# Kernel optimization log

Measured on AMD Instinct MI355X. Metric: run time of the kernel, lower is better.

Reference implementation:

```python
import jax, jax.numpy as jnp
import numpy as np

T, B, V, E, H = 256, 64, 10000, 400, 1152


def _n(k, shape, scale=0.05):
    return jax.random.normal(k, shape, jnp.float32) * scale


def setup_inputs() -> dict:
    key = jax.random.key(0)
    ks = jax.random.split(key, 32)
    inp = {}
    inp["x"] = jax.random.randint(ks[0], (T, B), 0, V)
    inp["h0"] = _n(ks[1], (B, H)); inp["h1"] = _n(ks[2], (B, H)); inp["h2"] = _n(ks[3], (B, E))
    inp["c0"] = _n(ks[4], (B, H)); inp["c1"] = _n(ks[5], (B, H)); inp["c2"] = _n(ks[6], (B, E))
    inp["emb"] = _n(ks[7], (V, E), 0.1)
    # layer i: (input_dim, output_dim): (E,H), (H,H), (H,E)
    sizes = [(E, H), (H, H), (H, E)]
    j = 8
    for i, (din, dout) in enumerate(sizes):
        inp[f"W_ih{i}"] = _n(ks[j], (4 * dout, din)); j += 1
        inp[f"W_hh{i}"] = _n(ks[j], (4 * dout, dout)); j += 1
        inp[f"b_ih{i}"] = _n(ks[j], (4 * dout,)); j += 1
        inp[f"b_hh{i}"] = _n(ks[j], (4 * dout,)); j += 1
    inp["dec_W"] = _n(ks[j], (V, E)); j += 1
    inp["dec_b"] = jnp.zeros((V,), jnp.float32)
    return inp


def lstm_cell(x, h, c, Wih, Whh, bih, bhh):
    # PyTorch LSTMCell: gates = x@Wih^T + bih + h@Whh^T + bhh, order i,f,g,o
    g = x @ Wih.T + h @ Whh.T + bih + bhh
    i, f, gg, o = jnp.split(g, 4, axis=-1)
    c2 = jax.nn.sigmoid(f) * c + jax.nn.sigmoid(i) * jnp.tanh(gg)
    h2 = jax.nn.sigmoid(o) * jnp.tanh(c2)
    return h2, c2


def reference(x, h0, h1, h2, c0, c1, c2, emb,
              W_ih0, W_hh0, b_ih0, b_hh0,
              W_ih1, W_hh1, b_ih1, b_hh1,
              W_ih2, W_hh2, b_ih2, b_hh2,
              dec_W, dec_b):
    xe = emb[x]  # [T, B, E]

    def step(carry, xt):
        a0, a1, a2, s0, s1, s2 = carry
        a0, s0 = lstm_cell(xt, a0, s0, W_ih0, W_hh0, b_ih0, b_hh0)
        a1, s1 = lstm_cell(a0, a1, s1, W_ih1, W_hh1, b_ih1, b_hh1)
        a2, s2 = lstm_cell(a1, a2, s2, W_ih2, W_hh2, b_ih2, b_hh2)
        return (a0, a1, a2, s0, s1, s2), a2

    _, out = jax.lax.scan(step, (h0, h1, h2, c0, c1, c2), xe)  # out: [T, B, E]
    decoded = out @ dec_W.T + dec_b  # [T, B, V]
    return decoded
```

## Files before the change

### kernel.cpp

```cpp
#include <hip/hip_runtime.h>
#include <hip/hip_bf16.h>

typedef __hip_bfloat16 bf16;
typedef __attribute__((ext_vector_type(8))) short short8;
typedef __attribute__((ext_vector_type(4))) float f32x4;

#define T_ 256
#define B_ 64
#define V_ 10000
#define E_ 400
#define H_ 1152
#define KU 2304
#define XW 416
#define KD 416
#define XET (XW*B_)
#define NBLK 169

#define MFMA16 __builtin_amdgcn_mfma_f32_16x16x32_bf16
#define ATL(p) __hip_atomic_load((p), __ATOMIC_RELAXED, __HIP_MEMORY_SCOPE_AGENT)
#define ATS(p, v) __hip_atomic_store((p), (v), __ATOMIC_RELAXED, __HIP_MEMORY_SCOPE_AGENT)
#define PIN(x) asm volatile("" : "+v"(x))


__global__ __launch_bounds__(256) void prep_wint(
    const float* __restrict__ s1, int w1,
    const float* __restrict__ s2, int off2, int w2, int Hl,
    bf16* __restrict__ dst, long total)
{
    long i = (long)blockIdx.x * 256 + threadIdx.x;
    if (i >= total) return;
    int r = (int)(i / KU), k = (int)(i % KU);
    int hcol = r >> 2, gate = r & 3;
    long srow = (long)gate * Hl + hcol;
    float v = 0.f;
    if (k < w1) v = s1[srow * w1 + k];
    else if (k >= off2 && k < off2 + w2) v = s2[srow * w2 + (k - off2)];
    dst[i] = __float2bfloat16(v);
}

__global__ __launch_bounds__(256) void prep_wcat(
    const float* __restrict__ s1, int w1,
    bf16* __restrict__ dst, int Ktot, long total)
{
    long i = (long)blockIdx.x * 256 + threadIdx.x;
    if (i >= total) return;
    int k = (int)(i % Ktot);
    long n = i / Ktot;
    dst[i] = __float2bfloat16(k < w1 ? s1[n * w1 + k] : 0.f);
}

__global__ __launch_bounds__(256) void bias_int(
    const float* __restrict__ a, const float* __restrict__ b,
    int Hl, float* __restrict__ d, int n)
{
    int r = blockIdx.x * 256 + threadIdx.x;
    if (r >= n) return;
    int hcol = r >> 2, gate = r & 3;
    d[r] = a[gate * Hl + hcol] + b[gate * Hl + hcol];
}

__global__ __launch_bounds__(256) void gather_xef(
    const int* __restrict__ x, const float* __restrict__ emb,
    bf16* __restrict__ XEf)
{
    long i = (long)blockIdx.x * 256 + threadIdx.x;
    if (i >= (long)T_ * B_ * XW) return;
    int k = (int)(i % XW);
    int b = (int)((i / XW) % B_);
    int t = (int)(i / ((long)XW * B_));
    float v = (k < E_) ? emb[(long)x[t * B_ + b] * E_ + k] : 0.f;
    XEf[(long)t * XET + (((k >> 3) * 64 + b) << 3) + (k & 7)] = __float2bfloat16(v);
}

__global__ __launch_bounds__(256) void copy_hf(
    const float* __restrict__ src, bf16* __restrict__ dst, int cols, int total)
{
    int i = blockIdx.x * 256 + threadIdx.x;
    if (i >= total) return;
    int k = i % cols, b = i / cols;
    dst[(((k >> 3) * 64 + b) << 3) + (k & 7)] = __float2bfloat16(src[(long)b * cols + k]);
}

__global__ __launch_bounds__(256) void copy_f32(
    const float* __restrict__ src, float* __restrict__ dst, int n)
{
    int i = blockIdx.x * 256 + threadIdx.x;
    if (i < n) dst[i] = src[i];
}

__device__ __forceinline__ void grid_bar(int* flags, int* gen, int phase) {
    asm volatile("s_waitcnt vmcnt(0)" ::: "memory");
    __syncthreads();
    if (blockIdx.x == 0) {
        if (threadIdx.x < 64) {
            const int ln = threadIdx.x;
            if (ln == 0) ATS(&flags[0], phase);
            for (;;) {
                int f0 = (ln       < NBLK) ? ATL(&flags[ln])       : phase;
                int f1 = (ln + 64  < NBLK) ? ATL(&flags[ln + 64])  : phase;
                int f2 = (ln + 128 < NBLK) ? ATL(&flags[ln + 128]) : phase;
                if (__all(f0 >= phase && f1 >= phase && f2 >= phase)) break;
                __builtin_amdgcn_s_sleep(1);
            }
            if (ln == 0) {
                ATS(gen, phase);
                __builtin_amdgcn_fence(__ATOMIC_ACQUIRE, "agent");
            }
        }
    } else {
        if (threadIdx.x == 0) {
            ATS(&flags[blockIdx.x], phase);
            while (ATL(gen) < phase)
                __builtin_amdgcn_s_sleep(1);
            __builtin_amdgcn_fence(__ATOMIC_ACQUIRE, "agent");
        }
    }
    __syncthreads();
    asm volatile("" ::: "memory");
}

struct Frag4 { short8 f0, f1, f2, f3; };

__global__ __launch_bounds__(512, 2) void awd_persistent(
    const bf16* __restrict__ XEf,
    const bf16* __restrict__ W0, const bf16* __restrict__ W1, const bf16* __restrict__ W2,
    const float* __restrict__ b0, const float* __restrict__ b1, const float* __restrict__ b2,
    bf16* H0f0, bf16* H0f1, bf16* H1f0, bf16* H1f1, bf16* H2f0, bf16* H2f1,
    float* c0, float* c1, float* c2, bf16* OUTB,
    int* flags, int* gen)
{
    __shared__ float gsm[2][4][64][65];
    __shared__ unsigned short hsm[64][24];
    const int bid = blockIdx.x;
    const int tid = threadIdx.x;
    const int lane = tid & 63;
    const int w8 = tid >> 6;
    const int lh = lane >> 4, l15 = lane & 15;
    const int boff8 = (lh * 64 + l15) * 8;

    int layer, grp;
    if (bid < 72)       { layer = 1; grp = bid; }
    else if (bid < 144) { layer = 0; grp = bid - 72; }
    else                { layer = 2; grp = bid - 144; }

    const bf16* Wp  = (layer == 0) ? W0 : (layer == 1) ? W1 : W2;
    const float* bias = (layer == 0) ? b0 : (layer == 1) ? b1 : b2;
    const float* cbuf = (layer == 0) ? c0 : (layer == 1) ? c1 : c2;
    const int Hl  = (layer == 2) ? 400 : 1152;
    const int bkt = (layer == 0) ? 13 : 36;
    const int nkt = (layer == 1) ? 72 : 49;
    const int KT  = (layer == 1) ? 9  : 7;
    const int kbase = w8 * KT;

    short8 wreg[9][4];
    #pragma unroll
    for (int u = 0; u < 9; ++u)
        if (u < KT) {
            #pragma unroll
            for (int rt = 0; rt < 4; ++rt) {
                int row = grp * 64 + rt * 16 + l15;
                int k   = (kbase + u) * 32 + lh * 8;
                wreg[u][rt] = *(const short8*)(Wp + (long)row * KU + k);
                PIN(wreg[u][rt]);
            }
        }

    float myb[2][4];
    #pragma unroll
    for (int e = 0; e < 2; ++e)
        #pragma unroll
        for (int g = 0; g < 4; ++g)
            myb[e][g] = bias[grp * 64 + (w8 + e * 8) * 4 + g];

    float creg[2];
    #pragma unroll
    for (int e = 0; e < 2; ++e)
        creg[e] = cbuf[(long)lane * Hl + grp * 16 + w8 + e * 8];

    for (int s = -1; s <= 256; ++s) {
        bool active = (layer == 0) ? (s <= 254)
                    : (layer == 1) ? (s >= 0 && s <= 255)
                                   : (s >= 1);
        if (active) {
            const int p = s & 1, q = p ^ 1;
            const bf16 *A1, *A2; bf16* hfW; bf16* ob = nullptr;
            if (layer == 0) {
                A1 = XEf + (long)(s + 1) * XET;
                A2 = p ? H0f1 : H0f0;
                hfW = q ? H0f1 : H0f0;
            } else if (layer == 1) {
                A1 = p ? H0f1 : H0f0;
                A2 = q ? H1f1 : H1f0;
                hfW = p ? H1f1 : H1f0;
            } else {
                A1 = q ? H1f1 : H1f0;
                A2 = p ? H2f1 : H2f0;
                hfW = q ? H2f1 : H2f0;
                ob = OUTB + (long)(s - 1) * B_ * XW;
            }

            auto loadf = [&](int u) -> Frag4 {
                const int ktg = kbase + u;
                const bf16* src; int ktL;
                if (ktg < bkt)      { src = A1; ktL = ktg; }
                else if (ktg < nkt) { src = A2; ktL = ktg - bkt; }
                else                { src = A1; ktL = 0; }
                const bf16* pB = src + ktL * 2048 + boff8;
                Frag4 r;
                r.f0 = *(const short8*)(pB);
                r.f1 = *(const short8*)(pB + 128);
                r.f2 = *(const short8*)(pB + 256);
                r.f3 = *(const short8*)(pB + 384);
                return r;
            };

            f32x4 acc[4][4];
            #pragma unroll
            for (int rt = 0; rt < 4; ++rt)
                #pragma unroll
                for (int m = 0; m < 4; ++m)
                    acc[rt][m] = (f32x4){0.f, 0.f, 0.f, 0.f};

            auto domfma = [&](int u, const Frag4& f) {
                #pragma unroll
                for (int rt = 0; rt < 4; ++rt) {
                    acc[rt][0] = MFMA16(wreg[u][rt], f.f0, acc[rt][0], 0, 0, 0);
                    acc[rt][1] = MFMA16(wreg[u][rt], f.f1, acc[rt][1], 0, 0, 0);
                    acc[rt][2] = MFMA16(wreg[u][rt], f.f2, acc[rt][2], 0, 0, 0);
                    acc[rt][3] = MFMA16(wreg[u][rt], f.f3, acc[rt][3], 0, 0, 0);
                }
            };

            #pragma unroll
            for (int u = 0; u < 9; ++u)
                if (u < KT) {
                    Frag4 f = loadf(u);
                    domfma(u, f);
                }

            #pragma unroll
            for (int rt = 0; rt < 4; ++rt)
                #pragma unroll
                for (int m = 0; m < 4; ++m)
                    #pragma unroll
                    for (int r = 0; r < 4; ++r)
                        gsm[w8 >> 2][w8 & 3][rt * 16 + lh * 4 + r][m * 16 + l15] = acc[rt][m][r];
            __syncthreads();

            #pragma unroll
            for (int e = 0; e < 2; ++e) {
                int b = lane;
                int cl = w8 + e * 8;
                float gv[4];
                #pragma unroll
                for (int g = 0; g < 4; ++g) {
                    float v = myb[e][g];
                    #pragma unroll
                    for (int kq = 0; kq < 4; ++kq)
                        v += gsm[0][kq][cl * 4 + g][b] + gsm[1][kq][cl * 4 + g][b];
                    gv[g] = v;
                }
                float c_old = creg[e];
                float i_s = 1.f / (1.f + expf(-gv[0]));
                float f_s = 1.f / (1.f + expf(-gv[1]));
                float o_s = 1.f / (1.f + expf(-gv[3]));
                float c_new = f_s * c_old + i_s * tanhf(gv[2]);
                float hval = o_s * tanhf(c_new);
                creg[e] = c_new;
                bf16 hb = __float2bfloat16(hval);
                unsigned short hbits;
                __builtin_memcpy(&hbits, &hb, 2);
                hsm[b][cl] = hbits;
            }
            __syncthreads();

            if (w8 < 2) {
                unsigned long long v0, v1;
                __builtin_memcpy(&v0, &hsm[lane][w8 * 8], 8);
                __builtin_memcpy(&v1, &hsm[lane][w8 * 8 + 4], 8);
                unsigned long long* qp =
                    (unsigned long long*)(hfW + (((long)grp * 2 + w8) * 64 + lane) * 8);
                ATS(qp, v0);
                ATS(qp + 1, v1);
            } else if (w8 == 2 && layer == 2) {
                short8 v0 = *(const short8*)&hsm[lane][0];
                short8 v1 = *(const short8*)&hsm[lane][8];
                *(short8*)(ob + (long)lane * XW + grp * 16) = v0;
                *(short8*)(ob + (long)lane * XW + grp * 16 + 8) = v1;
            }
        }
        grid_bar(flags, gen, s + 2);
    }
}

__global__ __launch_bounds__(256) void decoder(
    const bf16* __restrict__ A, const bf16* __restrict__ W,
    const float* __restrict__ bias, float* __restrict__ out)
{
    const int tid = threadIdx.x;
    const int lane = tid & 63;
    const int w = tid >> 6;
    const int mw = w >> 1, nw = w & 1;
    const int n0 = blockIdx.x * 128 + nw * 64;
    const int m0 = blockIdx.y * 128 + mw * 64;
    const int c16 = lane & 15;
    const int kg = lane >> 4;

    f32x4 acc[4][4];
    #pragma unroll
    for (int mi = 0; mi < 4; ++mi)
        #pragma unroll
        for (int ns = 0; ns < 4; ++ns)
            acc[mi][ns] = (f32x4){0.f, 0.f, 0.f, 0.f};

    int nrow[4];
    #pragma unroll
    for (int ns = 0; ns < 4; ++ns) {
        int n = n0 + ns * 16 + c16;
        nrow[ns] = (n < V_) ? n : (V_ - 1);
    }

    const bf16* arow = A + (long)(m0 + c16) * KD + kg * 8;
    #pragma unroll
    for (int kt = 0; kt < 13; ++kt) {
        short8 af[4], bf[4];
        #pragma unroll
        for (int mi = 0; mi < 4; ++mi)
            af[mi] = *(const short8*)(arow + (long)mi * 16 * KD + kt * 32);
        #pragma unroll
        for (int ns = 0; ns < 4; ++ns)
            bf[ns] = *(const short8*)(W + (long)nrow[ns] * KD + kt * 32 + kg * 8);
        #pragma unroll
        for (int mi = 0; mi < 4; ++mi)
            #pragma unroll
            for (int ns = 0; ns < 4; ++ns)
                acc[mi][ns] = MFMA16(af[mi], bf[ns], acc[mi][ns], 0, 0, 0);
    }

    #pragma unroll
    for (int mi = 0; mi < 4; ++mi)
        #pragma unroll
        for (int ns = 0; ns < 4; ++ns) {
            int col = n0 + ns * 16 + c16;
            if (col < V_) {
                float bv = bias[col];
                #pragma unroll
                for (int r = 0; r < 4; ++r) {
                    int row = m0 + mi * 16 + kg * 4 + r;
                    out[(size_t)row * V_ + col] = acc[mi][ns][r] + bv;
                }
            }
        }
}


extern "C" void kernel_launch(void* const* d_in, const int* in_sizes, int n_in,
                              void* d_out, int out_size, void* d_ws, size_t ws_size,
                              hipStream_t stream)
{
    const int*   x    = (const int*)d_in[0];
    const float* h0   = (const float*)d_in[1];
    const float* h1   = (const float*)d_in[2];
    const float* h2   = (const float*)d_in[3];
    const float* c0   = (const float*)d_in[4];
    const float* c1   = (const float*)d_in[5];
    const float* c2   = (const float*)d_in[6];
    const float* emb  = (const float*)d_in[7];
    const float* Wih0 = (const float*)d_in[8];
    const float* Whh0 = (const float*)d_in[9];
    const float* bih0 = (const float*)d_in[10];
    const float* bhh0 = (const float*)d_in[11];
    const float* Wih1 = (const float*)d_in[12];
    const float* Whh1 = (const float*)d_in[13];
    const float* bih1 = (const float*)d_in[14];
    const float* bhh1 = (const float*)d_in[15];
    const float* Wih2 = (const float*)d_in[16];
    const float* Whh2 = (const float*)d_in[17];
    const float* bih2 = (const float*)d_in[18];
    const float* bhh2 = (const float*)d_in[19];
    const float* decW = (const float*)d_in[20];
    const float* decb = (const float*)d_in[21];

    char* wsb = (char*)d_ws;
    size_t off = 0;
    auto alloc = [&](size_t bytes) -> void* {
        void* ptr = wsb + off;
        off = (off + bytes + 255) & ~(size_t)255;
        return ptr;
    };

    bf16* W0i = (bf16*)alloc((size_t)4608 * KU * 2);
    bf16* W1i = (bf16*)alloc((size_t)4608 * KU * 2);
    bf16* W2i = (bf16*)alloc((size_t)1600 * KU * 2);
    bf16* Wdc = (bf16*)alloc((size_t)V_ * KD * 2);
    float* b0i = (float*)alloc(4608 * 4);
    float* b1i = (float*)alloc(4608 * 4);
    float* b2i = (float*)alloc(1600 * 4);
    bf16* XEf = (bf16*)alloc((size_t)T_ * XET * 2);
    bf16* H0f0 = (bf16*)alloc((size_t)B_ * H_ * 2);
    bf16* H0f1 = (bf16*)alloc((size_t)B_ * H_ * 2);
    bf16* H1f0 = (bf16*)alloc((size_t)B_ * H_ * 2);
    bf16* H1f1 = (bf16*)alloc((size_t)B_ * H_ * 2);
    bf16* H2f0 = (bf16*)alloc((size_t)B_ * XW * 2);
    bf16* H2f1 = (bf16*)alloc((size_t)B_ * XW * 2);
    float* c0b = (float*)alloc((size_t)B_ * H_ * 4);
    float* c1b = (float*)alloc((size_t)B_ * H_ * 4);
    float* c2b = (float*)alloc((size_t)B_ * E_ * 4);
    bf16* OUTB = (bf16*)alloc((size_t)T_ * B_ * XW * 2);
    int* gbar = (int*)alloc(2048);

    auto cdiv = [](long a, long b) { return (int)((a + b - 1) / b); };

    hipMemsetAsync(gbar, 0, 2048, stream);

    prep_wint<<<cdiv(4608L * KU, 256), 256, 0, stream>>>(Wih0, 400,  Whh0, 416,  1152, 1152, W0i, 4608L * KU);
    prep_wint<<<cdiv(4608L * KU, 256), 256, 0, stream>>>(Wih1, 1152, Whh1, 1152, 1152, 1152, W1i, 4608L * KU);
    prep_wint<<<cdiv(1600L * KU, 256), 256, 0, stream>>>(Wih2, 1152, Whh2, 1152, 400,  400,  W2i, 1600L * KU);
    prep_wcat<<<cdiv((long)V_ * KD, 256), 256, 0, stream>>>(decW, 400, Wdc, KD, (long)V_ * KD);
    bias_int<<<cdiv(4608, 256), 256, 0, stream>>>(bih0, bhh0, 1152, b0i, 4608);
    bias_int<<<cdiv(4608, 256), 256, 0, stream>>>(bih1, bhh1, 1152, b1i, 4608);
    bias_int<<<cdiv(1600, 256), 256, 0, stream>>>(bih2, bhh2, 400,  b2i, 1600);
    gather_xef<<<cdiv((long)T_ * B_ * XW, 256), 256, 0, stream>>>(x, emb, XEf);

    hipMemsetAsync(H2f0, 0, (size_t)B_ * XW * 2, stream);
    hipMemsetAsync(H2f1, 0, (size_t)B_ * XW * 2, stream);
    hipMemsetAsync(OUTB, 0, (size_t)T_ * B_ * XW * 2, stream);

    copy_hf<<<cdiv(B_ * H_, 256), 256, 0, stream>>>(h0, H0f1, H_, B_ * H_);
    copy_hf<<<cdiv(B_ * H_, 256), 256, 0, stream>>>(h1, H1f1, H_, B_ * H_);
    copy_hf<<<cdiv(B_ * E_, 256), 256, 0, stream>>>(h2, H2f1, E_, B_ * E_);
    copy_f32<<<cdiv(B_ * H_, 256), 256, 0, stream>>>(c0, c0b, B_ * H_);
    copy_f32<<<cdiv(B_ * H_, 256), 256, 0, stream>>>(c1, c1b, B_ * H_);
    copy_f32<<<cdiv(B_ * E_, 256), 256, 0, stream>>>(c2, c2b, B_ * E_);

    {
        int* flags = gbar;
        int* gen   = gbar + 448;
        void* args[] = {
            (void*)&XEf, (void*)&W0i, (void*)&W1i, (void*)&W2i,
            (void*)&b0i, (void*)&b1i, (void*)&b2i,
            (void*)&H0f0, (void*)&H0f1, (void*)&H1f0, (void*)&H1f1,
            (void*)&H2f0, (void*)&H2f1,
            (void*)&c0b, (void*)&c1b, (void*)&c2b, (void*)&OUTB,
            (void*)&flags, (void*)&gen
        };
        hipLaunchCooperativeKernel((void*)awd_persistent, dim3(NBLK), dim3(512),
                                   args, 0, stream);
    }

    decoder<<<dim3((V_ + 127) / 128, (T_ * B_) / 128), 256, 0, stream>>>(
        OUTB, Wdc, decb, (float*)d_out);
}
```

Before: 3.157 ms.

## Replace global grid barrier with per-layer group flags and triple-buffered hidden states

Drops the single grid-wide barrier, which made every step wait for all 169 blocks. Each layer group now has a leader that collects its blocks' flags and publishes a per-layer generation counter. Blocks wait only on the layer counters they depend on, so layers can drift up to a step apart. To make that slack safe, hidden-state buffers go from double to triple buffering with a rotating read/write index. The cost is more polling and trickier ordering, and correctness depends on the dependency offsets and buffer rotation lining up.

```diff
diff --git a/kernel.cpp b/kernel.cpp
--- a/kernel.cpp
+++ b/kernel.cpp
@@ -88,46 +88,21 @@
     if (i < n) dst[i] = src[i];
 }
 
-__device__ __forceinline__ void grid_bar(int* flags, int* gen, int phase) {
-    asm volatile("s_waitcnt vmcnt(0)" ::: "memory");
-    __syncthreads();
-    if (blockIdx.x == 0) {
-        if (threadIdx.x < 64) {
-            const int ln = threadIdx.x;
-            if (ln == 0) ATS(&flags[0], phase);
-            for (;;) {
-                int f0 = (ln       < NBLK) ? ATL(&flags[ln])       : phase;
-                int f1 = (ln + 64  < NBLK) ? ATL(&flags[ln + 64])  : phase;
-                int f2 = (ln + 128 < NBLK) ? ATL(&flags[ln + 128]) : phase;
-                if (__all(f0 >= phase && f1 >= phase && f2 >= phase)) break;
-                __builtin_amdgcn_s_sleep(1);
-            }
-            if (ln == 0) {
-                ATS(gen, phase);
-                __builtin_amdgcn_fence(__ATOMIC_ACQUIRE, "agent");
-            }
-        }
-    } else {
-        if (threadIdx.x == 0) {
-            ATS(&flags[blockIdx.x], phase);
-            while (ATL(gen) < phase)
-                __builtin_amdgcn_s_sleep(1);
-            __builtin_amdgcn_fence(__ATOMIC_ACQUIRE, "agent");
-        }
-    }
-    __syncthreads();
-    asm volatile("" ::: "memory");
-}
-
 struct Frag4 { short8 f0, f1, f2, f3; };
+
+__device__ __forceinline__ void wait_ge(int* p, int v) {
+    while (ATL(p) < v) __builtin_amdgcn_s_sleep(1);
+}
 
 __global__ __launch_bounds__(512, 2) void awd_persistent(
     const bf16* __restrict__ XEf,
     const bf16* __restrict__ W0, const bf16* __restrict__ W1, const bf16* __restrict__ W2,
     const float* __restrict__ b0, const float* __restrict__ b1, const float* __restrict__ b2,
-    bf16* H0f0, bf16* H0f1, bf16* H1f0, bf16* H1f1, bf16* H2f0, bf16* H2f1,
+    bf16* H0a, bf16* H0b, bf16* H0c,
+    bf16* H1a, bf16* H1b, bf16* H1c,
+    bf16* H2a, bf16* H2b, bf16* H2c,
     float* c0, float* c1, float* c2, bf16* OUTB,
-    int* flags, int* gen)
+    int* flags, int* gd)
 {
     __shared__ float gsm[2][4][64][65];
     __shared__ unsigned short hsm[64][24];
@@ -143,6 +118,10 @@
     else if (bid < 144) { layer = 0; grp = bid - 72; }
     else                { layer = 2; grp = bid - 144; }
 
+    const bool isLeader = (bid == 0 || bid == 72 || bid == 144);
+    const int gbase = (layer == 1) ? 0 : (layer == 0) ? 72 : 144;
+    const int gcnt  = (layer == 2) ? 25 : 72;
+
     const bf16* Wp  = (layer == 0) ? W0 : (layer == 1) ? W1 : W2;
     const float* bias = (layer == 0) ? b0 : (layer == 1) ? b1 : b2;
     const float* cbuf = (layer == 0) ? c0 : (layer == 1) ? c1 : c2;
@@ -177,25 +156,40 @@
     for (int e = 0; e < 2; ++e)
         creg[e] = cbuf[(long)lane * Hl + grp * 16 + w8 + e * 8];
 
+    int rb = 0;
     for (int s = -1; s <= 256; ++s) {
+        const int ph = s + 2;
+        const int wb = (rb == 2) ? 0 : rb + 1;
+
+        if (tid == 0) {
+            if (layer == 0)      { wait_ge(&gd[0],  ph - 1); wait_ge(&gd[16], ph - 2); }
+            else if (layer == 1) { wait_ge(&gd[0],  ph - 1); wait_ge(&gd[16], ph - 1);
+                                   wait_ge(&gd[32], ph - 2); }
+            else                 { wait_ge(&gd[16], ph - 1); wait_ge(&gd[32], ph - 1); }
+            __builtin_amdgcn_fence(__ATOMIC_ACQUIRE, "agent");
+        }
+        __syncthreads();
+        asm volatile("" ::: "memory");
+
         bool active = (layer == 0) ? (s <= 254)
                     : (layer == 1) ? (s >= 0 && s <= 255)
                                    : (s >= 1);
         if (active) {
-            const int p = s & 1, q = p ^ 1;
+            const bf16* H0r = (rb == 0) ? H0a : (rb == 1) ? H0b : H0c;
+            const bf16* H1r = (rb == 0) ? H1a : (rb == 1) ? H1b : H1c;
+            const bf16* H2r = (rb == 0) ? H2a : (rb == 1) ? H2b : H2c;
+            bf16* H0w = (wb == 0) ? H0a : (wb == 1) ? H0b : H0c;
+            bf16* H1w = (wb == 0) ? H1a : (wb == 1) ? H1b : H1c;
+            bf16* H2w = (wb == 0) ? H2a : (wb == 1) ? H2b : H2c;
+
             const bf16 *A1, *A2; bf16* hfW; bf16* ob = nullptr;
             if (layer == 0) {
                 A1 = XEf + (long)(s + 1) * XET;
-                A2 = p ? H0f1 : H0f0;
-                hfW = q ? H0f1 : H0f0;
+                A2 = H0r; hfW = H0w;
             } else if (layer == 1) {
-                A1 = p ? H0f1 : H0f0;
-                A2 = q ? H1f1 : H1f0;
-                hfW = p ? H1f1 : H1f0;
+                A1 = H0r; A2 = H1r; hfW = H1w;
             } else {
-                A1 = q ? H1f1 : H1f0;
-                A2 = p ? H2f1 : H2f0;
-                hfW = q ? H2f1 : H2f0;
+                A1 = H1r; A2 = H2r; hfW = H2w;
                 ob = OUTB + (long)(s - 1) * B_ * XW;
             }
 
@@ -288,8 +282,23 @@
                 *(short8*)(ob + (long)lane * XW + grp * 16) = v0;
                 *(short8*)(ob + (long)lane * XW + grp * 16 + 8) = v1;
             }
+            asm volatile("s_waitcnt vmcnt(0)" ::: "memory");
         }
-        grid_bar(flags, gen, s + 2);
+        __syncthreads();
+
+        if (tid == 0) ATS(&flags[bid], ph);
+        if (isLeader && tid < 64) {
+            const int ln = tid;
+            for (;;) {
+                int f0 = (ln      < gcnt) ? ATL(&flags[gbase + ln])      : ph;
+                int f1 = (ln + 64 < gcnt) ? ATL(&flags[gbase + ln + 64]) : ph;
+                if (__all(f0 >= ph && f1 >= ph)) break;
+                __builtin_amdgcn_s_sleep(1);
+            }
+            if (ln == 0) ATS(&gd[layer * 16], ph);
+        }
+
+        rb = wb;
     }
 }
 
@@ -397,12 +406,10 @@
     float* b1i = (float*)alloc(4608 * 4);
     float* b2i = (float*)alloc(1600 * 4);
     bf16* XEf = (bf16*)alloc((size_t)T_ * XET * 2);
-    bf16* H0f0 = (bf16*)alloc((size_t)B_ * H_ * 2);
-    bf16* H0f1 = (bf16*)alloc((size_t)B_ * H_ * 2);
-    bf16* H1f0 = (bf16*)alloc((size_t)B_ * H_ * 2);
-    bf16* H1f1 = (bf16*)alloc((size_t)B_ * H_ * 2);
-    bf16* H2f0 = (bf16*)alloc((size_t)B_ * XW * 2);
-    bf16* H2f1 = (bf16*)alloc((size_t)B_ * XW * 2);
+    bf16* H0f[3], *H1f[3], *H2f[3];
+    for (int i = 0; i < 3; ++i) H0f[i] = (bf16*)alloc((size_t)B_ * H_ * 2);
+    for (int i = 0; i < 3; ++i) H1f[i] = (bf16*)alloc((size_t)B_ * H_ * 2);
+    for (int i = 0; i < 3; ++i) H2f[i] = (bf16*)alloc((size_t)B_ * XW * 2);
     float* c0b = (float*)alloc((size_t)B_ * H_ * 4);
     float* c1b = (float*)alloc((size_t)B_ * H_ * 4);
     float* c2b = (float*)alloc((size_t)B_ * E_ * 4);
@@ -422,27 +429,28 @@
     bias_int<<<cdiv(1600, 256), 256, 0, stream>>>(bih2, bhh2, 400,  b2i, 1600);
     gather_xef<<<cdiv((long)T_ * B_ * XW, 256), 256, 0, stream>>>(x, emb, XEf);
 
-    hipMemsetAsync(H2f0, 0, (size_t)B_ * XW * 2, stream);
-    hipMemsetAsync(H2f1, 0, (size_t)B_ * XW * 2, stream);
+    for (int i = 0; i < 3; ++i)
+        hipMemsetAsync(H2f[i], 0, (size_t)B_ * XW * 2, stream);
     hipMemsetAsync(OUTB, 0, (size_t)T_ * B_ * XW * 2, stream);
 
-    copy_hf<<<cdiv(B_ * H_, 256), 256, 0, stream>>>(h0, H0f1, H_, B_ * H_);
-    copy_hf<<<cdiv(B_ * H_, 256), 256, 0, stream>>>(h1, H1f1, H_, B_ * H_);
-    copy_hf<<<cdiv(B_ * E_, 256), 256, 0, stream>>>(h2, H2f1, E_, B_ * E_);
+    copy_hf<<<cdiv(B_ * H_, 256), 256, 0, stream>>>(h0, H0f[0], H_, B_ * H_);
+    copy_hf<<<cdiv(B_ * H_, 256), 256, 0, stream>>>(h1, H1f[1], H_, B_ * H_);
+    copy_hf<<<cdiv(B_ * E_, 256), 256, 0, stream>>>(h2, H2f[2], E_, B_ * E_);
     copy_f32<<<cdiv(B_ * H_, 256), 256, 0, stream>>>(c0, c0b, B_ * H_);
     copy_f32<<<cdiv(B_ * H_, 256), 256, 0, stream>>>(c1, c1b, B_ * H_);
     copy_f32<<<cdiv(B_ * E_, 256), 256, 0, stream>>>(c2, c2b, B_ * E_);
 
     {
         int* flags = gbar;
-        int* gen   = gbar + 448;
+        int* gd    = gbar + 256;
         void* args[] = {
             (void*)&XEf, (void*)&W0i, (void*)&W1i, (void*)&W2i,
             (void*)&b0i, (void*)&b1i, (void*)&b2i,
-            (void*)&H0f0, (void*)&H0f1, (void*)&H1f0, (void*)&H1f1,
-            (void*)&H2f0, (void*)&H2f1,
+            (void*)&H0f[0], (void*)&H0f[1], (void*)&H0f[2],
+            (void*)&H1f[0], (void*)&H1f[1], (void*)&H1f[2],
+            (void*)&H2f[0], (void*)&H2f[1], (void*)&H2f[2],
             (void*)&c0b, (void*)&c1b, (void*)&c2b, (void*)&OUTB,
-            (void*)&flags, (void*)&gen
+            (void*)&flags, (void*)&gd
         };
         hipLaunchCooperativeKernel((void*)awd_persistent, dim3(NBLK), dim3(512),
                                    args, 0, stream);
```

Result: no change. 3.220 ms (+2.0%).
